# Kernel optimization log

Measured on AMD Instinct MI355X. Metric: run time of the kernel, lower is better.

## Reference

```python
import jax, jax.numpy as jnp
import numpy as np

NU = 1.0  # degrees of freedom of the Student-t / Tsallis softmax


def setup_inputs() -> dict:
    key = jax.random.key(0)
    k1, k2, k3, k4 = jax.random.split(key, 4)
    B, Nx, Nh, Ny = 8192, 2048, 512, 1024
    x = jax.random.normal(k1, (B, Nx), dtype=jnp.float32)
    W_fc = jax.random.normal(k2, (Nh, Nx), dtype=jnp.float32) * (1.0 / np.sqrt(Nx))
    b_fc = jax.random.normal(k3, (Nh,), dtype=jnp.float32) * 0.01
    W_q = jax.random.normal(k4, (Ny, Nh), dtype=jnp.float32) * (1.0 / np.sqrt(Nh))
    return {"x": x, "W_fc": W_fc, "b_fc": b_fc, "W_q": W_q}


def reference(x, W_fc, b_fc, W_q):
    # x: [B, Nx] -> relu -> Linear(Nx, Nh) -> relu
    h = jax.nn.relu(jax.nn.relu(x) @ W_fc.T + b_fc)  # [B, Nh]
    # Quadratic layer: squared Euclidean distance to each class prototype.
    # ||h - w_j||^2 = ||h||^2 - 2 h.w_j + ||w_j||^2  (avoids [B, Ny, Nh] tensor)
    d = (jnp.sum(h * h, axis=-1, keepdims=True)
         - 2.0 * (h @ W_q.T)
         + jnp.sum(W_q * W_q, axis=-1))  # [B, Ny]
    d = jnp.maximum(d, 0.0)  # guard tiny negatives from fp cancellation
    # LogTSoftmax: p_j \propto (1 + d_j/nu)^{-(nu+1)/2}
    t = (-(NU + 1.0) / 2.0) * jnp.log1p(d / NU)  # [B, Ny]
    return t - jax.scipy.special.logsumexp(t, axis=-1, keepdims=True)
```

## Files before the change

kernel.cpp:

```cpp
#include <hip/hip_runtime.h>
#include <stdint.h>
#include <stddef.h>

#define B_ROWS 8192
#define NX 2048
#define NH 512
#define NY 1024

#define X_ELEMS (B_ROWS * NX)
#define EW_ELEMS (X_ELEMS + NH * NX)
#define EW_BLOCKS (EW_ELEMS / (8 * 256))
#define WQ_BLOCKS (NY / 4)

typedef __attribute__((ext_vector_type(8))) short bf16x8;
typedef __attribute__((ext_vector_type(4))) float f32x4;

static __device__ __forceinline__ unsigned short f2bf(float f) {
    union { float f; unsigned int u; } c; c.f = f;
    unsigned int r = 0x7FFFu + ((c.u >> 16) & 1u);
    return (unsigned short)((c.u + r) >> 16);
}

static __device__ __forceinline__ void glld16(const void* g, void* l) {
    __builtin_amdgcn_global_load_lds(
        (const __attribute__((address_space(1))) unsigned int*)g,
        (__attribute__((address_space(3))) unsigned int*)l, 16, 0, 0);
}

__global__ __launch_bounds__(256) void prep_kernel(const float* __restrict__ x,
                                                   const float* __restrict__ wfc,
                                                   const float* __restrict__ wq,
                                                   unsigned short* __restrict__ xb,
                                                   unsigned short* __restrict__ wfcb,
                                                   unsigned short* __restrict__ wqb,
                                                   float* __restrict__ wqsq,
                                                   float* __restrict__ hsq) {
    const int bid = blockIdx.x;
    const int tid = threadIdx.x;
    if (bid < EW_BLOCKS) {
        size_t idx = ((size_t)bid * 256 + tid) * 8;
        if (idx < (size_t)X_ELEMS) {
            float4 a = *(const float4*)&x[idx];
            float4 b = *(const float4*)&x[idx + 4];
            bf16x8 o;
            o[0] = (short)f2bf(fmaxf(a.x, 0.f)); o[1] = (short)f2bf(fmaxf(a.y, 0.f));
            o[2] = (short)f2bf(fmaxf(a.z, 0.f)); o[3] = (short)f2bf(fmaxf(a.w, 0.f));
            o[4] = (short)f2bf(fmaxf(b.x, 0.f)); o[5] = (short)f2bf(fmaxf(b.y, 0.f));
            o[6] = (short)f2bf(fmaxf(b.z, 0.f)); o[7] = (short)f2bf(fmaxf(b.w, 0.f));
            *(bf16x8*)&xb[idx] = o;
        } else {
            size_t off = idx - X_ELEMS;
            float4 a = *(const float4*)&wfc[off];
            float4 b = *(const float4*)&wfc[off + 4];
            bf16x8 o;
            o[0] = (short)f2bf(a.x); o[1] = (short)f2bf(a.y);
            o[2] = (short)f2bf(a.z); o[3] = (short)f2bf(a.w);
            o[4] = (short)f2bf(b.x); o[5] = (short)f2bf(b.y);
            o[6] = (short)f2bf(b.z); o[7] = (short)f2bf(b.w);
            *(bf16x8*)&wfcb[off] = o;
        }
    } else {
        const int b2 = bid - EW_BLOCKS;
        const int lane = tid & 63;
        const int row = b2 * 4 + (tid >> 6);
        const float* p = wq + (size_t)row * NH + lane * 8;
        float4 a = *(const float4*)p;
        float4 b = *(const float4*)(p + 4);
        bf16x8 o;
        o[0] = (short)f2bf(a.x); o[1] = (short)f2bf(a.y);
        o[2] = (short)f2bf(a.z); o[3] = (short)f2bf(a.w);
        o[4] = (short)f2bf(b.x); o[5] = (short)f2bf(b.y);
        o[6] = (short)f2bf(b.z); o[7] = (short)f2bf(b.w);
        *(bf16x8*)&wqb[(size_t)row * NH + lane * 8] = o;
        float s = a.x*a.x + a.y*a.y + a.z*a.z + a.w*a.w
                + b.x*b.x + b.y*b.y + b.z*b.z + b.w*b.w;
        #pragma unroll
        for (int off = 32; off > 0; off >>= 1) s += __shfl_xor(s, off);
        if (lane == 0) wqsq[row] = s;
        if (tid < 32) hsq[b2 * 32 + tid] = 0.0f;
    }
}

__global__ __launch_bounds__(128, 1) void gemm1_kernel(const unsigned short* __restrict__ xb,
                                                       const unsigned short* __restrict__ wfcb,
                                                       const float* __restrict__ b_fc,
                                                       unsigned short* __restrict__ hb,
                                                       float* __restrict__ hsq) {
    __shared__ unsigned short Bs[2 * 2 * 128 * 64];

    const int tid = threadIdx.x;
    const int lane = tid & 63;
    const int wave = tid >> 6;
    const int quad = lane >> 4;
    const int r = lane & 15;

    const int bid = blockIdx.x;
    const int n0 = ((bid >> 3) & 3) * 128;
    const int m0 = (((bid & 7) << 4) | (bid >> 5)) * 64;

    f32x4 acc[4][4];
    #pragma unroll
    for (int i = 0; i < 4; ++i)
        #pragma unroll
        for (int j = 0; j < 4; ++j) acc[i][j] = (f32x4)(0.0f);

    const int lrow = lane >> 3;
    const int gch = (lane & 7) ^ lrow;
    const char* wfB = (const char*)wfcb;
    char* BsB = (char*)Bs;
    const int xk = r & 7;

    auto stage = [&](int buf, int k0) {
        #pragma unroll
        for (int t = 0; t < 2; ++t) {
            #pragma unroll
            for (int c = 0; c < 8; ++c) {
                int R0 = wave * 64 + c * 8;
                glld16(wfB + (size_t)(n0 + R0 + lrow) * (NX * 2) + (k0 + t * 64) * 2 + gch * 16,
                       BsB + buf * 32768 + t * 16384 + R0 * 128);
            }
        }
    };

    stage(0, 0);
    for (int it = 0; it < NX / 128; ++it) {
        const int k0 = it * 128;
        __syncthreads();
        if (it + 1 < NX / 128) stage((it + 1) & 1, k0 + 128);
        const char* bufp = BsB + (it & 1) * 32768;
        #pragma unroll
        for (int t = 0; t < 2; ++t) {
            #pragma unroll
            for (int s = 0; s < 2; ++s) {
                const int ch = ((s * 4 + quad) ^ xk) * 16;
                bf16x8 af[4], bfv[4];
                #pragma unroll
                for (int i = 0; i < 4; ++i)
                    af[i] = *(const bf16x8*)&xb[(size_t)(m0 + i * 16 + r) * NX + k0 + (t * 2 + s) * 32 + quad * 8];
                #pragma unroll
                for (int j = 0; j < 4; ++j)
                    bfv[j] = *(const bf16x8*)(bufp + t * 16384 + (wave * 64 + j * 16 + r) * 128 + ch);
                #pragma unroll
                for (int i = 0; i < 4; ++i)
                    #pragma unroll
                    for (int j = 0; j < 4; ++j)
                        acc[i][j] = __builtin_amdgcn_mfma_f32_16x16x32_bf16(af[i], bfv[j], acc[i][j], 0, 0, 0);
            }
        }
    }

    float p[4][4];
    #pragma unroll
    for (int i = 0; i < 4; ++i)
        #pragma unroll
        for (int rr = 0; rr < 4; ++rr) p[i][rr] = 0.0f;

    #pragma unroll
    for (int i = 0; i < 4; ++i) {
        #pragma unroll
        for (int j = 0; j < 4; ++j) {
            int col = n0 + wave * 64 + j * 16 + r;
            float bias = b_fc[col];
            #pragma unroll
            for (int rr = 0; rr < 4; ++rr) {
                int row = m0 + i * 16 + quad * 4 + rr;
                float v = fmaxf(acc[i][j][rr] + bias, 0.0f);
                hb[(size_t)row * NH + col] = f2bf(v);
                p[i][rr] += v * v;
            }
        }
    }
    #pragma unroll
    for (int mask = 1; mask < 16; mask <<= 1) {
        #pragma unroll
        for (int i = 0; i < 4; ++i)
            #pragma unroll
            for (int rr = 0; rr < 4; ++rr)
                p[i][rr] += __shfl_xor(p[i][rr], mask);
    }
    if (r == 0) {
        #pragma unroll
        for (int i = 0; i < 4; ++i)
            #pragma unroll
            for (int rr = 0; rr < 4; ++rr)
                atomicAdd(&hsq[m0 + i * 16 + quad * 4 + rr], p[i][rr]);
    }
}

__global__ __launch_bounds__(256, 2) void gemm2_kernel(const unsigned short* __restrict__ hb,
                                                       const unsigned short* __restrict__ wqb,
                                                       const float* __restrict__ hsq,
                                                       const float* __restrict__ wqsq,
                                                       float* __restrict__ out) {
    __shared__ unsigned short As[2 * 128 * 64];
    __shared__ unsigned short Bs[2 * 128 * 64];

    const int tid = threadIdx.x;
    const int lane = tid & 63;
    const int wave = tid >> 6;
    const int wm = wave >> 1, wn = wave & 1;
    const int quad = lane >> 4;
    const int r = lane & 15;

    const int bid = blockIdx.x;
    const int n0 = ((bid >> 3) & 7) * 128;
    const int m0 = (((bid & 7) << 3) | (bid >> 6)) * 128;

    f32x4 acc[4][4];
    #pragma unroll
    for (int i = 0; i < 4; ++i)
        #pragma unroll
        for (int j = 0; j < 4; ++j) acc[i][j] = (f32x4)(0.0f);

    const int lrow = lane >> 3;
    const int gch = (lane & 7) ^ lrow;
    const char* hbB = (const char*)hb;
    const char* wqB = (const char*)wqb;
    char* AsB = (char*)As;
    char* BsB = (char*)Bs;
    const int xk = r & 7;

    auto stage = [&](int buf, int k0) {
        #pragma unroll
        for (int c = 0; c < 4; ++c) {
            int R0 = wave * 32 + c * 8;
            glld16(hbB + (size_t)(m0 + R0 + lrow) * (NH * 2) + k0 * 2 + gch * 16,
                   AsB + buf * 16384 + R0 * 128);
            glld16(wqB + (size_t)(n0 + R0 + lrow) * (NH * 2) + k0 * 2 + gch * 16,
                   BsB + buf * 16384 + R0 * 128);
        }
    };

    stage(0, 0);
    for (int it = 0; it < NH / 64; ++it) {
        const int k0 = it * 64;
        __syncthreads();
        if (it + 1 < NH / 64) stage((it + 1) & 1, k0 + 64);
        const char* ap = AsB + (it & 1) * 16384 + (wm * 64 + r) * 128;
        const char* bp = BsB + (it & 1) * 16384 + (wn * 64 + r) * 128;
        #pragma unroll
        for (int s = 0; s < 2; ++s) {
            const int ch = ((s * 4 + quad) ^ xk) * 16;
            bf16x8 af[4], bfv[4];
            #pragma unroll
            for (int i = 0; i < 4; ++i) af[i] = *(const bf16x8*)(ap + i * 16 * 128 + ch);
            #pragma unroll
            for (int j = 0; j < 4; ++j) bfv[j] = *(const bf16x8*)(bp + j * 16 * 128 + ch);
            #pragma unroll
            for (int i = 0; i < 4; ++i)
                #pragma unroll
                for (int j = 0; j < 4; ++j)
                    acc[i][j] = __builtin_amdgcn_mfma_f32_16x16x32_bf16(af[i], bfv[j], acc[i][j], 0, 0, 0);
        }
    }

    float hs[4][4];
    #pragma unroll
    for (int i = 0; i < 4; ++i)
        #pragma unroll
        for (int rr = 0; rr < 4; ++rr)
            hs[i][rr] = hsq[m0 + wm * 64 + i * 16 + quad * 4 + rr];

    #pragma unroll
    for (int i = 0; i < 4; ++i) {
        #pragma unroll
        for (int j = 0; j < 4; ++j) {
            int col = n0 + wn * 64 + j * 16 + r;
            float wq = wqsq[col];
            #pragma unroll
            for (int rr = 0; rr < 4; ++rr) {
                int row = m0 + wm * 64 + i * 16 + quad * 4 + rr;
                float d = hs[i][rr] - 2.0f * acc[i][j][rr] + wq;
                d = fmaxf(d, 0.0f);
                out[(size_t)row * NY + col] = -__logf(1.0f + d);
            }
        }
    }
}

__global__ __launch_bounds__(256) void lse_kernel(float* __restrict__ out) {
    __shared__ float reds[4];
    const int tid = threadIdx.x;
    const int lane = tid & 63;
    const int wave = tid >> 6;
    float* p = out + (size_t)blockIdx.x * NY;
    float4 v = ((const float4*)p)[tid];
    float s = __expf(v.x) + __expf(v.y) + __expf(v.z) + __expf(v.w);
    #pragma unroll
    for (int off = 32; off > 0; off >>= 1) s += __shfl_xor(s, off);
    if (lane == 0) reds[wave] = s;
    __syncthreads();
    float lse = __logf(reds[0] + reds[1] + reds[2] + reds[3]);
    v.x -= lse; v.y -= lse; v.z -= lse; v.w -= lse;
    ((float4*)p)[tid] = v;
}

extern "C" void kernel_launch(void* const* d_in, const int* in_sizes, int n_in,
                              void* d_out, int out_size, void* d_ws, size_t ws_size,
                              hipStream_t stream) {
    const float* x    = (const float*)d_in[0];
    const float* W_fc = (const float*)d_in[1];
    const float* b_fc = (const float*)d_in[2];
    const float* W_q  = (const float*)d_in[3];
    float* out = (float*)d_out;

    char* ws = (char*)d_ws;
    unsigned short* xb   = (unsigned short*)(ws);
    unsigned short* wfcb = (unsigned short*)(ws + 33554432);
    unsigned short* wqb  = (unsigned short*)(ws + 35651584);
    float*          wqsq = (float*)(ws + 36700160);
    unsigned short* hb   = (unsigned short*)(ws + 36704256);
    float*          hsq  = (float*)(ws + 45092864);

    prep_kernel<<<EW_BLOCKS + WQ_BLOCKS, 256, 0, stream>>>(x, W_fc, W_q, xb, wfcb, wqb, wqsq, hsq);
    gemm1_kernel<<<512, 128, 0, stream>>>(xb, wfcb, b_fc, hb, hsq);
    gemm2_kernel<<<512, 256, 0, stream>>>(hb, wqb, hsq, wqsq, out);
    lse_kernel<<<B_ROWS, 256, 0, stream>>>(out);
}
```

Before: 193.4 us.

## Split GEMM1 over K into two halves with 128x128 LDS tiles and a reduce kernel

GEMM1 is restructured as a split-K GEMM. Each of 512 blocks now computes a 128x128 tile over half of K, staging both A and B through LDS with async loads, where before A was read straight from global memory with 64x128 tiles. The fp32 partials go into the output buffer, and a new reduce kernel sums the two halves, adds the bias, applies ReLU, writes bf16 h and computes the row norms. This removes the atomics and the zeroing of hsq, and it raises per-block data reuse and occupancy. In exchange it adds a 16 MB fp32 partial write and read-back plus an extra kernel launch.

New measurement: 169.5 us. 1.14x faster.

```diff
diff --git a/kernel.cpp b/kernel.cpp
--- a/kernel.cpp
+++ b/kernel.cpp
@@ -33,8 +33,7 @@
                                                    unsigned short* __restrict__ xb,
                                                    unsigned short* __restrict__ wfcb,
                                                    unsigned short* __restrict__ wqb,
-                                                   float* __restrict__ wqsq,
-                                                   float* __restrict__ hsq) {
+                                                   float* __restrict__ wqsq) {
     const int bid = blockIdx.x;
     const int tid = threadIdx.x;
     if (bid < EW_BLOCKS) {
@@ -77,26 +76,27 @@
         #pragma unroll
         for (int off = 32; off > 0; off >>= 1) s += __shfl_xor(s, off);
         if (lane == 0) wqsq[row] = s;
-        if (tid < 32) hsq[b2 * 32 + tid] = 0.0f;
-    }
-}
-
-__global__ __launch_bounds__(128, 1) void gemm1_kernel(const unsigned short* __restrict__ xb,
+    }
+}
+
+__global__ __launch_bounds__(256, 2) void gemm1_kernel(const unsigned short* __restrict__ xb,
                                                        const unsigned short* __restrict__ wfcb,
-                                                       const float* __restrict__ b_fc,
-                                                       unsigned short* __restrict__ hb,
-                                                       float* __restrict__ hsq) {
-    __shared__ unsigned short Bs[2 * 2 * 128 * 64];
+                                                       float* __restrict__ partial) {
+    __shared__ unsigned short As[2 * 128 * 64];
+    __shared__ unsigned short Bs[2 * 128 * 64];
 
     const int tid = threadIdx.x;
     const int lane = tid & 63;
     const int wave = tid >> 6;
+    const int wm = wave >> 1, wn = wave & 1;
     const int quad = lane >> 4;
     const int r = lane & 15;
 
     const int bid = blockIdx.x;
     const int n0 = ((bid >> 3) & 3) * 128;
-    const int m0 = (((bid & 7) << 4) | (bid >> 5)) * 64;
+    const int kh = (bid >> 5) & 1;
+    const int m0 = (((bid & 7) << 3) | (bid >> 6)) * 128;
+    const int kbase = kh * (NX / 2);
 
     f32x4 acc[4][4];
     #pragma unroll
@@ -106,85 +106,91 @@
 
     const int lrow = lane >> 3;
     const int gch = (lane & 7) ^ lrow;
+    const char* xbB = (const char*)xb;
     const char* wfB = (const char*)wfcb;
+    char* AsB = (char*)As;
     char* BsB = (char*)Bs;
     const int xk = r & 7;
 
     auto stage = [&](int buf, int k0) {
         #pragma unroll
-        for (int t = 0; t < 2; ++t) {
-            #pragma unroll
-            for (int c = 0; c < 8; ++c) {
-                int R0 = wave * 64 + c * 8;
-                glld16(wfB + (size_t)(n0 + R0 + lrow) * (NX * 2) + (k0 + t * 64) * 2 + gch * 16,
-                       BsB + buf * 32768 + t * 16384 + R0 * 128);
-            }
+        for (int c = 0; c < 4; ++c) {
+            int R0 = wave * 32 + c * 8;
+            glld16(xbB + (size_t)(m0 + R0 + lrow) * (NX * 2) + k0 * 2 + gch * 16,
+                   AsB + buf * 16384 + R0 * 128);
+            glld16(wfB + (size_t)(n0 + R0 + lrow) * (NX * 2) + k0 * 2 + gch * 16,
+                   BsB + buf * 16384 + R0 * 128);
         }
     };
 
-    stage(0, 0);
-    for (int it = 0; it < NX / 128; ++it) {
-        const int k0 = it * 128;
+    stage(0, kbase);
+    #pragma unroll 1
+    for (int it = 0; it < 16; ++it) {
+        const int k0 = kbase + it * 64;
         __syncthreads();
-        if (it + 1 < NX / 128) stage((it + 1) & 1, k0 + 128);
-        const char* bufp = BsB + (it & 1) * 32768;
-        #pragma unroll
-        for (int t = 0; t < 2; ++t) {
-            #pragma unroll
-            for (int s = 0; s < 2; ++s) {
-                const int ch = ((s * 4 + quad) ^ xk) * 16;
-                bf16x8 af[4], bfv[4];
-                #pragma unroll
-                for (int i = 0; i < 4; ++i)
-                    af[i] = *(const bf16x8*)&xb[(size_t)(m0 + i * 16 + r) * NX + k0 + (t * 2 + s) * 32 + quad * 8];
+        if (it + 1 < 16) stage((it + 1) & 1, k0 + 64);
+        const char* ap = AsB + (it & 1) * 16384 + (wm * 64 + r) * 128;
+        const char* bp = BsB + (it & 1) * 16384 + (wn * 64 + r) * 128;
+        #pragma unroll
+        for (int s = 0; s < 2; ++s) {
+            const int ch = ((s * 4 + quad) ^ xk) * 16;
+            bf16x8 af[4], bfv[4];
+            #pragma unroll
+            for (int i = 0; i < 4; ++i) af[i] = *(const bf16x8*)(ap + i * 16 * 128 + ch);
+            #pragma unroll
+            for (int j = 0; j < 4; ++j) bfv[j] = *(const bf16x8*)(bp + j * 16 * 128 + ch);
+            #pragma unroll
+            for (int i = 0; i < 4; ++i)
                 #pragma unroll
                 for (int j = 0; j < 4; ++j)
-                    bfv[j] = *(const bf16x8*)(bufp + t * 16384 + (wave * 64 + j * 16 + r) * 128 + ch);
-                #pragma unroll
-                for (int i = 0; i < 4; ++i)
-                    #pragma unroll
-                    for (int j = 0; j < 4; ++j)
-                        acc[i][j] = __builtin_amdgcn_mfma_f32_16x16x32_bf16(af[i], bfv[j], acc[i][j], 0, 0, 0);
+                    acc[i][j] = __builtin_amdgcn_mfma_f32_16x16x32_bf16(af[i], bfv[j], acc[i][j], 0, 0, 0);
+        }
+    }
+
+    float* pout = partial + (size_t)kh * (B_ROWS * NH);
+    #pragma unroll
+    for (int i = 0; i < 4; ++i) {
+        #pragma unroll
+        for (int j = 0; j < 4; ++j) {
+            int col = n0 + wn * 64 + j * 16 + r;
+            #pragma unroll
+            for (int rr = 0; rr < 4; ++rr) {
+                int row = m0 + wm * 64 + i * 16 + quad * 4 + rr;
+                pout[(size_t)row * NH + col] = acc[i][j][rr];
             }
         }
     }
-
-    float p[4][4];
-    #pragma unroll
-    for (int i = 0; i < 4; ++i)
-        #pragma unroll
-        for (int rr = 0; rr < 4; ++rr) p[i][rr] = 0.0f;
-
-    #pragma unroll
-    for (int i = 0; i < 4; ++i) {
-        #pragma unroll
-        for (int j = 0; j < 4; ++j) {
-            int col = n0 + wave * 64 + j * 16 + r;
-            float bias = b_fc[col];
-            #pragma unroll
-            for (int rr = 0; rr < 4; ++rr) {
-                int row = m0 + i * 16 + quad * 4 + rr;
-                float v = fmaxf(acc[i][j][rr] + bias, 0.0f);
-                hb[(size_t)row * NH + col] = f2bf(v);
-                p[i][rr] += v * v;
-            }
-        }
-    }
-    #pragma unroll
-    for (int mask = 1; mask < 16; mask <<= 1) {
-        #pragma unroll
-        for (int i = 0; i < 4; ++i)
-            #pragma unroll
-            for (int rr = 0; rr < 4; ++rr)
-                p[i][rr] += __shfl_xor(p[i][rr], mask);
-    }
-    if (r == 0) {
-        #pragma unroll
-        for (int i = 0; i < 4; ++i)
-            #pragma unroll
-            for (int rr = 0; rr < 4; ++rr)
-                atomicAdd(&hsq[m0 + i * 16 + quad * 4 + rr], p[i][rr]);
-    }
+}
+
+__global__ __launch_bounds__(256) void reduce_kernel(const float* __restrict__ partial,
+                                                     const float* __restrict__ b_fc,
+                                                     unsigned short* __restrict__ hb,
+                                                     float* __restrict__ hsq) {
+    const int tid = threadIdx.x;
+    const int lane = tid & 63;
+    const int row = blockIdx.x * 4 + (tid >> 6);
+    const int c0 = lane * 8;
+    const float* p0 = partial + (size_t)row * NH + c0;
+    const float* p1 = partial + (size_t)(B_ROWS * NH) + (size_t)row * NH + c0;
+    float4 a0 = *(const float4*)p0;
+    float4 a1 = *(const float4*)(p0 + 4);
+    float4 b0 = *(const float4*)p1;
+    float4 b1 = *(const float4*)(p1 + 4);
+    float4 f0 = *(const float4*)&b_fc[c0];
+    float4 f1 = *(const float4*)&b_fc[c0 + 4];
+    float h[8];
+    h[0] = fmaxf(a0.x + b0.x + f0.x, 0.f); h[1] = fmaxf(a0.y + b0.y + f0.y, 0.f);
+    h[2] = fmaxf(a0.z + b0.z + f0.z, 0.f); h[3] = fmaxf(a0.w + b0.w + f0.w, 0.f);
+    h[4] = fmaxf(a1.x + b1.x + f1.x, 0.f); h[5] = fmaxf(a1.y + b1.y + f1.y, 0.f);
+    h[6] = fmaxf(a1.z + b1.z + f1.z, 0.f); h[7] = fmaxf(a1.w + b1.w + f1.w, 0.f);
+    bf16x8 o;
+    float s = 0.f;
+    #pragma unroll
+    for (int i = 0; i < 8; ++i) { o[i] = (short)f2bf(h[i]); s += h[i] * h[i]; }
+    *(bf16x8*)&hb[(size_t)row * NH + c0] = o;
+    #pragma unroll
+    for (int off = 32; off > 0; off >>= 1) s += __shfl_xor(s, off);
+    if (lane == 0) hsq[row] = s;
 }
 
 __global__ __launch_bounds__(256, 2) void gemm2_kernel(const unsigned short* __restrict__ hb,
@@ -232,6 +238,7 @@
     };
 
     stage(0, 0);
+    #pragma unroll 1
     for (int it = 0; it < NH / 64; ++it) {
         const int k0 = it * 64;
         __syncthreads();
@@ -312,8 +319,11 @@
     unsigned short* hb   = (unsigned short*)(ws + 36704256);
     float*          hsq  = (float*)(ws + 45092864);
 
-    prep_kernel<<<EW_BLOCKS + WQ_BLOCKS, 256, 0, stream>>>(x, W_fc, W_q, xb, wfcb, wqb, wqsq, hsq);
-    gemm1_kernel<<<512, 128, 0, stream>>>(xb, wfcb, b_fc, hb, hsq);
+    float* partial = out;
+
+    prep_kernel<<<EW_BLOCKS + WQ_BLOCKS, 256, 0, stream>>>(x, W_fc, W_q, xb, wfcb, wqb, wqsq);
+    gemm1_kernel<<<512, 256, 0, stream>>>(xb, wfcb, partial);
+    reduce_kernel<<<B_ROWS / 4, 256, 0, stream>>>(partial, b_fc, hb, hsq);
     gemm2_kernel<<<512, 256, 0, stream>>>(hb, wqb, hsq, wqsq, out);
     lse_kernel<<<B_ROWS, 256, 0, stream>>>(out);
 }
```

## Restructure gemm1 into 128x128 tiles with split-K wave groups and LDS-staged A

Applied to the files above, without the earlier changes.

gemm1 now uses 512-thread blocks covering 128x128 output tiles instead of 128-thread blocks on 64x128 tiles. Two groups of four waves each take half of the K dimension and combine their partial sums through LDS before the bias, ReLU and norm epilogue. The x operand is now staged into swizzled LDS with async global-to-LDS loads instead of being read straight from global memory per MFMA. This aims for better operand reuse and more waves per CU, at the cost of an extra LDS reduction pass, fewer blocks, and higher LDS use that may limit occupancy.

Measured after the change: 166.5 us. 13.9% less time.

```diff
diff --git a/kernel.cpp b/kernel.cpp
--- a/kernel.cpp
+++ b/kernel.cpp
@@ -81,22 +81,27 @@
     }
 }
 
-__global__ __launch_bounds__(128, 1) void gemm1_kernel(const unsigned short* __restrict__ xb,
+__global__ __launch_bounds__(512, 2) void gemm1_kernel(const unsigned short* __restrict__ xb,
                                                        const unsigned short* __restrict__ wfcb,
                                                        const float* __restrict__ b_fc,
                                                        unsigned short* __restrict__ hb,
                                                        float* __restrict__ hsq) {
-    __shared__ unsigned short Bs[2 * 2 * 128 * 64];
+    __shared__ unsigned char smem[65536];
+    unsigned char* AsB = smem;
+    unsigned char* BsB = smem + 32768;
 
     const int tid = threadIdx.x;
     const int lane = tid & 63;
-    const int wave = tid >> 6;
+    const int grp = tid >> 8;
+    const int wave = (tid >> 6) & 3;
+    const int wm = wave >> 1, wn = wave & 1;
     const int quad = lane >> 4;
     const int r = lane & 15;
 
     const int bid = blockIdx.x;
     const int n0 = ((bid >> 3) & 3) * 128;
-    const int m0 = (((bid & 7) << 4) | (bid >> 5)) * 64;
+    const int m0 = (((bid & 7) << 3) | (bid >> 5)) * 128;
+    const int kbase = grp * (NX / 2);
 
     f32x4 acc[4][4];
     #pragma unroll
@@ -104,86 +109,98 @@
         #pragma unroll
         for (int j = 0; j < 4; ++j) acc[i][j] = (f32x4)(0.0f);
 
-    const int lrow = lane >> 3;
-    const int gch = (lane & 7) ^ lrow;
+    const int lrow = lane >> 2;
+    const int gch = (lane & 3) ^ ((lrow >> 1) & 3);
+    const char* xbB = (const char*)xb;
     const char* wfB = (const char*)wfcb;
-    char* BsB = (char*)Bs;
-    const int xk = r & 7;
+    const int fsw = (quad ^ ((r >> 1) & 3)) * 16;
 
     auto stage = [&](int buf, int k0) {
-        #pragma unroll
-        for (int t = 0; t < 2; ++t) {
-            #pragma unroll
-            for (int c = 0; c < 8; ++c) {
-                int R0 = wave * 64 + c * 8;
-                glld16(wfB + (size_t)(n0 + R0 + lrow) * (NX * 2) + (k0 + t * 64) * 2 + gch * 16,
-                       BsB + buf * 32768 + t * 16384 + R0 * 128);
+        const int sb = grp * 16384 + buf * 8192;
+        #pragma unroll
+        for (int c = 0; c < 2; ++c) {
+            int R0 = wave * 32 + c * 16;
+            glld16(xbB + (size_t)(m0 + R0 + lrow) * (NX * 2) + k0 * 2 + gch * 16,
+                   AsB + sb + R0 * 64);
+            glld16(wfB + (size_t)(n0 + R0 + lrow) * (NX * 2) + k0 * 2 + gch * 16,
+                   BsB + sb + R0 * 64);
+        }
+    };
+
+    stage(0, kbase);
+    #pragma unroll 1
+    for (int it = 0; it < 32; ++it) {
+        __syncthreads();
+        if (it + 1 < 32) stage((it + 1) & 1, kbase + it * 32 + 32);
+        const unsigned char* ab = AsB + grp * 16384 + (it & 1) * 8192;
+        const unsigned char* bb = BsB + grp * 16384 + (it & 1) * 8192;
+        bf16x8 af[4], bfv[4];
+        #pragma unroll
+        for (int i = 0; i < 4; ++i)
+            af[i] = *(const bf16x8*)(ab + (wm * 64 + i * 16 + r) * 64 + fsw);
+        #pragma unroll
+        for (int j = 0; j < 4; ++j)
+            bfv[j] = *(const bf16x8*)(bb + (wn * 64 + j * 16 + r) * 64 + fsw);
+        #pragma unroll
+        for (int i = 0; i < 4; ++i)
+            #pragma unroll
+            for (int j = 0; j < 4; ++j)
+                acc[i][j] = __builtin_amdgcn_mfma_f32_16x16x32_bf16(af[i], bfv[j], acc[i][j], 0, 0, 0);
+    }
+
+    float* smemF = (float*)smem;
+    __syncthreads();
+    if (grp == 1) {
+        #pragma unroll
+        for (int i = 0; i < 4; ++i) {
+            #pragma unroll
+            for (int j = 0; j < 4; ++j) {
+                int cl = wn * 64 + j * 16 + r;
+                int rowb = wm * 64 + i * 16 + quad * 4;
+                *(f32x4*)(smemF + cl * 128 + (rowb ^ ((cl & 7) << 2))) = acc[i][j];
             }
         }
-    };
-
-    stage(0, 0);
-    for (int it = 0; it < NX / 128; ++it) {
-        const int k0 = it * 128;
-        __syncthreads();
-        if (it + 1 < NX / 128) stage((it + 1) & 1, k0 + 128);
-        const char* bufp = BsB + (it & 1) * 32768;
-        #pragma unroll
-        for (int t = 0; t < 2; ++t) {
-            #pragma unroll
-            for (int s = 0; s < 2; ++s) {
-                const int ch = ((s * 4 + quad) ^ xk) * 16;
-                bf16x8 af[4], bfv[4];
+    }
+    __syncthreads();
+    if (grp == 0) {
+        float p[4][4];
+        #pragma unroll
+        for (int i = 0; i < 4; ++i)
+            #pragma unroll
+            for (int rr = 0; rr < 4; ++rr) p[i][rr] = 0.0f;
+
+        #pragma unroll
+        for (int i = 0; i < 4; ++i) {
+            #pragma unroll
+            for (int j = 0; j < 4; ++j) {
+                int cl = wn * 64 + j * 16 + r;
+                int rowb = wm * 64 + i * 16 + quad * 4;
+                f32x4 o = *(const f32x4*)(smemF + cl * 128 + (rowb ^ ((cl & 7) << 2)));
+                int col = n0 + cl;
+                float bias = b_fc[col];
                 #pragma unroll
-                for (int i = 0; i < 4; ++i)
-                    af[i] = *(const bf16x8*)&xb[(size_t)(m0 + i * 16 + r) * NX + k0 + (t * 2 + s) * 32 + quad * 8];
+                for (int rr = 0; rr < 4; ++rr) {
+                    float v = fmaxf(acc[i][j][rr] + o[rr] + bias, 0.0f);
+                    hb[(size_t)(m0 + rowb + rr) * NH + col] = f2bf(v);
+                    p[i][rr] += v * v;
+                }
+            }
+        }
+        #pragma unroll
+        for (int mask = 1; mask < 16; mask <<= 1) {
+            #pragma unroll
+            for (int i = 0; i < 4; ++i)
                 #pragma unroll
-                for (int j = 0; j < 4; ++j)
-                    bfv[j] = *(const bf16x8*)(bufp + t * 16384 + (wave * 64 + j * 16 + r) * 128 + ch);
+                for (int rr = 0; rr < 4; ++rr)
+                    p[i][rr] += __shfl_xor(p[i][rr], mask);
+        }
+        if (r == 0) {
+            #pragma unroll
+            for (int i = 0; i < 4; ++i)
                 #pragma unroll
-                for (int i = 0; i < 4; ++i)
-                    #pragma unroll
-                    for (int j = 0; j < 4; ++j)
-                        acc[i][j] = __builtin_amdgcn_mfma_f32_16x16x32_bf16(af[i], bfv[j], acc[i][j], 0, 0, 0);
-            }
-        }
-    }
-
-    float p[4][4];
-    #pragma unroll
-    for (int i = 0; i < 4; ++i)
-        #pragma unroll
-        for (int rr = 0; rr < 4; ++rr) p[i][rr] = 0.0f;
-
-    #pragma unroll
-    for (int i = 0; i < 4; ++i) {
-        #pragma unroll
-        for (int j = 0; j < 4; ++j) {
-            int col = n0 + wave * 64 + j * 16 + r;
-            float bias = b_fc[col];
-            #pragma unroll
-            for (int rr = 0; rr < 4; ++rr) {
-                int row = m0 + i * 16 + quad * 4 + rr;
-                float v = fmaxf(acc[i][j][rr] + bias, 0.0f);
-                hb[(size_t)row * NH + col] = f2bf(v);
-                p[i][rr] += v * v;
-            }
-        }
-    }
-    #pragma unroll
-    for (int mask = 1; mask < 16; mask <<= 1) {
-        #pragma unroll
-        for (int i = 0; i < 4; ++i)
-            #pragma unroll
-            for (int rr = 0; rr < 4; ++rr)
-                p[i][rr] += __shfl_xor(p[i][rr], mask);
-    }
-    if (r == 0) {
-        #pragma unroll
-        for (int i = 0; i < 4; ++i)
-            #pragma unroll
-            for (int rr = 0; rr < 4; ++rr)
-                atomicAdd(&hsq[m0 + i * 16 + quad * 4 + rr], p[i][rr]);
+                for (int rr = 0; rr < 4; ++rr)
+                    atomicAdd(&hsq[m0 + wm * 64 + i * 16 + quad * 4 + rr], p[i][rr]);
+        }
     }
 }
 
@@ -232,6 +249,7 @@
     };
 
     stage(0, 0);
+    #pragma unroll 1
     for (int it = 0; it < NH / 64; ++it) {
         const int k0 = it * 64;
         __syncthreads();
@@ -313,7 +331,7 @@
     float*          hsq  = (float*)(ws + 45092864);
 
     prep_kernel<<<EW_BLOCKS + WQ_BLOCKS, 256, 0, stream>>>(x, W_fc, W_q, xb, wfcb, wqb, wqsq, hsq);
-    gemm1_kernel<<<512, 128, 0, stream>>>(xb, wfcb, b_fc, hb, hsq);
+    gemm1_kernel<<<256, 512, 0, stream>>>(xb, wfcb, b_fc, hb, hsq);
     gemm2_kernel<<<512, 256, 0, stream>>>(hb, wqb, hsq, wqsq, out);
     lse_kernel<<<B_ROWS, 256, 0, stream>>>(out);
 }
```
